# Performance work log

Hardware: AMD Instinct MI355X
Metric: run time of the kernel (lower is better)

The kernel has to match this reference:

```python
import jax, jax.numpy as jnp
import numpy as np

B, S, N, IN_DIM = 64, 12, 170, 1
E, L, C, H, OUT = 128, 4, 2, 8, 1
OFFSET, PAD = 0, 1          # seq_offset=0 -> Conv2d padding (0,1)
LOOKUP, MAXLEN = 0, 100
EPS = 1e-5


def _shift(x, s):
    """y[:, i] = x[:, i+s] along axis 1, zero padded."""
    if s == 0:
        return x
    z = jnp.zeros_like(x[:, :abs(s)])
    if s > 0:
        return jnp.concatenate([x[:, s:], z], axis=1)
    return jnp.concatenate([z, x[:, :s]], axis=1)


def _masked_conv_diag(x, w):
    """Diagonal of Conv2d(kernel=(1,3), pad=(0,PAD)) applied to the causally
    masked repeated tensor, computed directly without the O(B*S*S*E) blowup:
      out[b,i] = sum_k W[:,:,k] @ (mask(i, i+k-PAD) * x[b, i+k-PAD])
    where mask(i,j) = (j <= i) or (j < OFFSET)."""
    i = jnp.arange(x.shape[1])
    out = None
    for k in range(3):
        s = k - PAD
        term = jnp.einsum('bse,oe->bso', _shift(x, s), w[:, :, k])
        if s > 0:  # only future taps can be masked out
            term = term * (i + s < OFFSET).astype(x.dtype)[None, :, None]
        out = term if out is None else out + term
    return out


def _conv1d_k3(x, w, b):
    """Conv1d over the seq dim, kernel 3, padding 1, with bias. x:[b,s,e]."""
    out = b
    for k in range(3):
        out = out + jnp.einsum('bse,oe->bso', _shift(x, k - 1), w[:, :, k])
    return out


def _layer_norm(x, g, b):
    m = jnp.mean(x, -1, keepdims=True)
    v = jnp.mean((x - m) ** 2, -1, keepdims=True)
    return (x - m) * jax.lax.rsqrt(v + EPS) * g + b


def _mha(q_in, kv_in, w, b, mask=None):
    dh = E // H
    q = (q_in @ w[0] + b[0]).reshape(q_in.shape[0], q_in.shape[1], H, dh)
    k = (kv_in @ w[1] + b[1]).reshape(kv_in.shape[0], kv_in.shape[1], H, dh)
    v = (kv_in @ w[2] + b[2]).reshape(kv_in.shape[0], kv_in.shape[1], H, dh)
    s = jnp.einsum('bqhd,bkhd->bhqk', q, k) * np.float32(1.0 / np.sqrt(dh))
    if mask is not None:
        s = jnp.where(mask[None, None], s, jnp.float32(-1e9))
    a = jax.nn.softmax(s, axis=-1)
    o = jnp.einsum('bhqk,bkhd->bqhd', a, v).reshape(q_in.shape[0], q_in.shape[1], E)
    return o @ w[3] + b[3]


def setup_inputs() -> dict:
    key = jax.random.key(0)
    ks = jax.random.split(key, 16)

    def nrm(k, shape, scale=0.05):
        return scale * jax.random.normal(k, shape, dtype=jnp.float32)

    # sinusoidal positional table, length MAXLEN
    pos = np.arange(MAXLEN)[:, None].astype(np.float32)
    div = np.exp(-np.log(10000.0) * np.arange(0, E, 2) / E).astype(np.float32)
    pe = np.zeros((MAXLEN, E), np.float32)
    pe[:, 0::2] = np.sin(pos * div)
    pe[:, 1::2] = np.cos(pos * div)

    return {
        'x': jax.random.normal(ks[0], (B, S, N, IN_DIM), jnp.float32),
        'enc_x': jax.random.normal(ks[1], (C, B * N, S, E), jnp.float32),
        'tgt_mask': jnp.tril(jnp.ones((S, S), bool)),
        'emb_w': nrm(ks[2], (IN_DIM, E), 1.0),
        'emb_b': jnp.zeros((E,), jnp.float32),
        'pe': jnp.asarray(pe),
        'conv_q_w': nrm(ks[3], (L, E, E, 3)),
        'conv_k_w': nrm(ks[4], (L, C, E, E, 3)),
        'conv_k_b': jnp.zeros((L, C, E), jnp.float32),
        'sa_w': nrm(ks[5], (L, 4, E, E)),
        'sa_b': jnp.zeros((L, 4, E), jnp.float32),
        'ca_w': nrm(ks[6], (L, C, 4, E, E)),
        'ca_b': jnp.zeros((L, C, 4, E), jnp.float32),
        'ff_w1': nrm(ks[7], (L, E, 4 * E)),
        'ff_b1': jnp.zeros((L, 4 * E), jnp.float32),
        'ff_w2': nrm(ks[8], (L, 4 * E, E)),
        'ff_b2': jnp.zeros((L, E), jnp.float32),
        'ln_g': jnp.ones((L, 3, E), jnp.float32),
        'ln_b': jnp.zeros((L, 3, E), jnp.float32),
        'fc_w': nrm(ks[9], (E, OUT)),
        'fc_b': jnp.zeros((OUT,), jnp.float32),
    }


def reference(x, enc_x, tgt_mask, emb_w, emb_b, pe, conv_q_w, conv_k_w, conv_k_b,
              sa_w, sa_b, ca_w, ca_b, ff_w1, ff_b1, ff_w2, ff_b2, ln_g, ln_b,
              fc_w, fc_b):
    h = x @ emb_w + emb_b                                    # [B,S,N,E]
    h = jnp.transpose(h, (1, 0, 2, 3)).reshape(S, B * N, E)  # [S,B*N,E]
    h = jnp.transpose(h, (1, 0, 2))                          # [B*N,S,E]
    h = h + pe[LOOKUP:LOOKUP + S]
    for l in range(L):
        # local trends: causal masked-conv query (the fused diagonal)
        h = _masked_conv_diag(h, conv_q_w[l])
        enc_list = [_conv1d_k3(enc_x[i], conv_k_w[l, i], conv_k_b[l, i])
                    for i in range(C)]
        # decoder block: self-attn -> cross-attn (avg over features) -> FFN
        h = _layer_norm(h + _mha(h, h, sa_w[l], sa_b[l], tgt_mask),
                        ln_g[l, 0], ln_b[l, 0])
        cross = sum(_mha(h, enc_list[i], ca_w[l, i], ca_b[l, i])
                    for i in range(C)) / C
        h = _layer_norm(h + cross, ln_g[l, 1], ln_b[l, 1])
        f = jax.nn.relu(h @ ff_w1[l] + ff_b1[l]) @ ff_w2[l] + ff_b2[l]
        h = _layer_norm(h + f, ln_g[l, 2], ln_b[l, 2])
    out = h @ fc_w + fc_b                                    # [B*N,S,OUT]
    out = jnp.transpose(out, (1, 0, 2)).reshape(S, B, N, OUT)
    return jnp.transpose(out, (1, 0, 2, 3))                  # [B,S,N,OUT]
```

## Files before the change

### kernel.cpp

```cpp
#include <hip/hip_runtime.h>


#define B_   64
#define S_   12
#define N_   170
#define BN_  (B_*N_)
#define E_   128
#define L_   4
#define C_   2
#define H_   8
#define DH_  16
#define FF_  512
#define EPS_ 1e-5f
#define THREADS 256

typedef unsigned short u16;
typedef __attribute__((ext_vector_type(4))) float f32x4;
typedef __attribute__((ext_vector_type(8))) u16   us8;
typedef __attribute__((ext_vector_type(4))) u16   us4;
typedef __attribute__((ext_vector_type(8))) __bf16 bf16x8;
union FragU { us8 u; bf16x8 b; };

__device__ __forceinline__ u16 f2bf(float f) {
    __bf16 h = (__bf16)f;
    return __builtin_bit_cast(u16, h);
}
__device__ __forceinline__ float bf2f(u16 s) {
    return __builtin_bit_cast(float, (unsigned)s << 16);
}

__global__ void k_wpack(const float* __restrict__ cq, const float* __restrict__ sa,
                        const float* __restrict__ ck, const float* __restrict__ ca,
                        const float* __restrict__ f1, const float* __restrict__ f2,
                        u16* __restrict__ wp) {
    int f  = blockIdx.x * 256 + threadIdx.x;
    int l  = f / 57344, fl = f % 57344;
    const float* src; int sk, so, KS, q;
    if (fl < 4096)        { int tap = fl >> 11; q = fl & 2047; KS = 4;
                            src = cq + (size_t)l*49152 + tap;            sk = 3;   so = 384; }
    else if (fl < 12288)  { int j = (fl - 4096) >> 11; q = fl & 2047; KS = 4;
                            src = sa + (size_t)(l*4 + j)*16384;          sk = 128; so = 1;   }
    else if (fl < 24576)  { int ct = (fl - 12288) >> 11; q = fl & 2047; KS = 4;
                            int ci = ct / 3, tap = ct % 3;
                            src = ck + (size_t)(l*2 + ci)*49152 + tap;   sk = 3;   so = 384; }
    else if (fl < 40960)  { int cj = (fl - 24576) >> 11; q = fl & 2047; KS = 4;
                            src = ca + (size_t)(l*8 + cj)*16384;         sk = 128; so = 1;   }
    else if (fl < 49152)  { q = fl - 40960; KS = 4;
                            src = f1 + (size_t)l*65536;                  sk = 512; so = 1;   }
    else                  { q = fl - 49152; KS = 16;
                            src = f2 + (size_t)l*65536;                  sk = 128; so = 1;   }
    int lane = q & 63, tt = q >> 6;
    int ks = tt % KS, ntile = tt / KS;
    int k0 = ks*32 + ((lane >> 4) << 3);
    int o  = ntile*16 + (lane & 15);
    us8 w;
    #pragma unroll
    for (int i = 0; i < 8; i++) w[i] = f2bf(src[(size_t)(k0 + i)*sk + (size_t)o*so]);
    *(us8*)(wp + (size_t)f*8) = w;
}

__device__ __forceinline__ void stage24(const float* __restrict__ src, u16* dst, int t) {
    #pragma unroll
    for (int it = 0; it < 3; it++) {
        int i = t + it*THREADS;
        const f32x4 v = ((const f32x4*)src)[i];
        int elem = i << 2;
        int srow = elem >> 7;
        int g = srow / 12, s = srow - g*12;
        int row = g*16 + s;
        int colb = (elem & 127) << 1;
        us4 w; w[0] = f2bf(v[0]); w[1] = f2bf(v[1]); w[2] = f2bf(v[2]); w[3] = f2bf(v[3]);
        *(us4*)((char*)dst + (((row << 8) + colb) ^ ((row & 7) << 4))) = w;
    }
}

__device__ __forceinline__ void stage24_embed(const float* __restrict__ x,
    const float* __restrict__ ew, const float* __restrict__ eb,
    const float* __restrict__ pe, int bn0, u16* dst, int t) {
    #pragma unroll
    for (int it = 0; it < 3; it++) {
        int i = t + it*THREADS;
        int elem = i << 2;
        int srow = elem >> 7;
        int g = srow / 12, s = srow - g*12;
        int row = g*16 + s;
        int col = elem & 127;
        int bn = bn0 + g, b = bn / N_, n = bn - b*N_;
        float xv = x[(b*S_ + s)*N_ + n];
        const f32x4 w  = *(const f32x4*)(ew + col);
        const f32x4 bb = *(const f32x4*)(eb + col);
        const f32x4 p  = *(const f32x4*)(pe + s*E_ + col);
        us4 o; o[0] = f2bf(xv*w[0] + bb[0] + p[0]); o[1] = f2bf(xv*w[1] + bb[1] + p[1]);
               o[2] = f2bf(xv*w[2] + bb[2] + p[2]); o[3] = f2bf(xv*w[3] + bb[3] + p[3]);
        *(us4*)((char*)dst + (((row << 8) + (col << 1)) ^ ((row & 7) << 4))) = o;
    }
}

__device__ __forceinline__ void acc_init(f32x4 (&acc)[2][2], const float* bias, int wave, int lane) {
    #pragma unroll
    for (int nt = 0; nt < 2; nt++) {
        float bv = bias ? bias[(wave*2 + nt)*16 + (lane & 15)] : 0.f;
        #pragma unroll
        for (int mt = 0; mt < 2; mt++) {
            acc[mt][nt][0] = bv; acc[mt][nt][1] = bv; acc[mt][nt][2] = bv; acc[mt][nt][3] = bv;
        }
    }
}

__device__ __forceinline__ bf16x8 ldA(const u16* A, int row, int colb) {
    FragU fu; fu.u = *(const us8*)((const char*)A + (((row << 8) + colb) ^ ((row & 7) << 4)));
    return fu.b;
}

template<int KSTOT>
__device__ __forceinline__ void gemm24(const u16* A, const us8* __restrict__ WP, int ksOff,
                                       f32x4 (&acc)[2][2], int wave, int lane) {
    #pragma unroll
    for (int ks = 0; ks < 4; ks++) {
        int colb = (ks*32 + ((lane >> 4) << 3)) << 1;
        bf16x8 a[2];
        #pragma unroll
        for (int mt = 0; mt < 2; mt++) a[mt] = ldA(A, mt*16 + (lane & 15), colb);
        #pragma unroll
        for (int nt = 0; nt < 2; nt++) {
            FragU fb; fb.u = WP[((wave*2 + nt)*KSTOT + ksOff + ks)*64 + lane];
            #pragma unroll
            for (int mt = 0; mt < 2; mt++)
                acc[mt][nt] = __builtin_amdgcn_mfma_f32_16x16x32_bf16(a[mt], fb.b, acc[mt][nt], 0, 0, 0);
        }
    }
}

__device__ __forceinline__ void gemm24_rows(const u16* A, const u16* ZR, const int (&sr)[2],
                                            const us8* __restrict__ WP,
                                            f32x4 (&acc)[2][2], int wave, int lane) {
    #pragma unroll
    for (int ks = 0; ks < 4; ks++) {
        int colb = (ks*32 + ((lane >> 4) << 3)) << 1;
        bf16x8 a[2];
        #pragma unroll
        for (int mt = 0; mt < 2; mt++) {
            const char* p = (sr[mt] >= 0)
                ? (const char*)A + (((sr[mt] << 8) + colb) ^ ((sr[mt] & 7) << 4))
                : (const char*)ZR + colb;
            FragU fu; fu.u = *(const us8*)p;
            a[mt] = fu.b;
        }
        #pragma unroll
        for (int nt = 0; nt < 2; nt++) {
            FragU fb; fb.u = WP[((wave*2 + nt)*4 + ks)*64 + lane];
            #pragma unroll
            for (int mt = 0; mt < 2; mt++)
                acc[mt][nt] = __builtin_amdgcn_mfma_f32_16x16x32_bf16(a[mt], fb.b, acc[mt][nt], 0, 0, 0);
        }
    }
}

__device__ __forceinline__ void gemm24_x3(const u16* A,
        const us8* __restrict__ B0, const us8* __restrict__ B1, const us8* __restrict__ B2,
        f32x4 (&c0)[2][2], f32x4 (&c1)[2][2], f32x4 (&c2)[2][2], int wave, int lane) {
    #pragma unroll
    for (int ks = 0; ks < 4; ks++) {
        int colb = (ks*32 + ((lane >> 4) << 3)) << 1;
        bf16x8 a[2];
        #pragma unroll
        for (int mt = 0; mt < 2; mt++) a[mt] = ldA(A, mt*16 + (lane & 15), colb);
        #pragma unroll
        for (int nt = 0; nt < 2; nt++) {
            int bi = ((wave*2 + nt)*4 + ks)*64 + lane;
            FragU f0, f1, f2; f0.u = B0[bi]; f1.u = B1[bi]; f2.u = B2[bi];
            #pragma unroll
            for (int mt = 0; mt < 2; mt++) {
                c0[mt][nt] = __builtin_amdgcn_mfma_f32_16x16x32_bf16(a[mt], f0.b, c0[mt][nt], 0, 0, 0);
                c1[mt][nt] = __builtin_amdgcn_mfma_f32_16x16x32_bf16(a[mt], f1.b, c1[mt][nt], 0, 0, 0);
                c2[mt][nt] = __builtin_amdgcn_mfma_f32_16x16x32_bf16(a[mt], f2.b, c2[mt][nt], 0, 0, 0);
            }
        }
    }
}

__device__ __forceinline__ void gemm24_x2(const u16* A,
        const us8* __restrict__ B0, const us8* __restrict__ B1,
        f32x4 (&c0)[2][2], f32x4 (&c1)[2][2], int wave, int lane) {
    #pragma unroll
    for (int ks = 0; ks < 4; ks++) {
        int colb = (ks*32 + ((lane >> 4) << 3)) << 1;
        bf16x8 a[2];
        #pragma unroll
        for (int mt = 0; mt < 2; mt++) a[mt] = ldA(A, mt*16 + (lane & 15), colb);
        #pragma unroll
        for (int nt = 0; nt < 2; nt++) {
            int bi = ((wave*2 + nt)*4 + ks)*64 + lane;
            FragU f0, f1; f0.u = B0[bi]; f1.u = B1[bi];
            #pragma unroll
            for (int mt = 0; mt < 2; mt++) {
                c0[mt][nt] = __builtin_amdgcn_mfma_f32_16x16x32_bf16(a[mt], f0.b, c0[mt][nt], 0, 0, 0);
                c1[mt][nt] = __builtin_amdgcn_mfma_f32_16x16x32_bf16(a[mt], f1.b, c1[mt][nt], 0, 0, 0);
            }
        }
    }
}

template<bool RELU>
__device__ __forceinline__ void acc_store_bf(const f32x4 (&acc)[2][2], u16* Bp, int wave, int lane) {
    #pragma unroll
    for (int mt = 0; mt < 2; mt++)
    #pragma unroll
    for (int nt = 0; nt < 2; nt++)
    #pragma unroll
    for (int r = 0; r < 4; r++) {
        int row = mt*16 + ((lane >> 4) << 2) + r;
        int col = (wave*2 + nt)*16 + (lane & 15);
        float v = acc[mt][nt][r];
        if (RELU) v = fmaxf(v, 0.f);
        *(u16*)((char*)Bp + (((row << 8) + (col << 1)) ^ ((row & 7) << 4))) = f2bf(v);
    }
}

__device__ __forceinline__ void ld16(const u16* Bf, int row, int colb, float* o16) {
    int x = (row & 7) << 4;
    int base = (row << 8) + colb;
    us8 u0 = *(const us8*)((const char*)Bf + (base ^ x));
    us8 u1 = *(const us8*)((const char*)Bf + ((base + 16) ^ x));
    #pragma unroll
    for (int d = 0; d < 8; d++) { o16[d] = bf2f(u0[d]); o16[8+d] = bf2f(u1[d]); }
}

template<bool MASK>
__device__ __forceinline__ void attn24(u16* QA, const u16* KB, const u16* VB, int t) {
    if (t < 192) {
        int g = t / 96, rem = t % 96;
        int hh = rem / 12, qi = rem % 12;
        int hb2 = hh << 5;
        int rq = g*16 + qi;
        float qv[16]; ld16(QA, rq, hb2, qv);
        float sc[12]; float mx = -1e30f;
        #pragma unroll
        for (int j = 0; j < 12; j++) {
            float kv[16]; ld16(KB, g*16 + j, hb2, kv);
            float s = 0.f;
            #pragma unroll
            for (int d = 0; d < 16; d++) s += qv[d]*kv[d];
            s *= 0.25f;
            if (MASK && j > qi) s = -1e30f;
            sc[j] = s; mx = fmaxf(mx, s);
        }
        float sum = 0.f;
        #pragma unroll
        for (int j = 0; j < 12; j++) { sc[j] = __expf(sc[j] - mx); sum += sc[j]; }
        float inv = 1.f/sum;
        float ov[16];
        #pragma unroll
        for (int d = 0; d < 16; d++) ov[d] = 0.f;
        #pragma unroll
        for (int j = 0; j < 12; j++) {
            float vv[16]; ld16(VB, g*16 + j, hb2, vv);
            #pragma unroll
            for (int d = 0; d < 16; d++) ov[d] += sc[j]*vv[d];
        }
        int x = (rq & 7) << 4;
        us8 w0, w1;
        #pragma unroll
        for (int d = 0; d < 8; d++) { w0[d] = f2bf(ov[d]*inv); w1[d] = f2bf(ov[8+d]*inv); }
        *(us8*)((char*)QA + (((rq << 8) + hb2) ^ x))      = w0;
        *(us8*)((char*)QA + (((rq << 8) + hb2 + 16) ^ x)) = w1;
    }
}

__device__ __forceinline__ void ln_inreg(f32x4 (&v)[2][2], float* lnbuf,
                                         const float* __restrict__ g, const float* __restrict__ bb,
                                         int wave, int lane) {
    float gc[2], bc[2];
    #pragma unroll
    for (int nt = 0; nt < 2; nt++) {
        int col = (wave*2 + nt)*16 + (lane & 15);
        gc[nt] = g[col]; bc[nt] = bb[col];
    }
    #pragma unroll
    for (int mt = 0; mt < 2; mt++)
    #pragma unroll
    for (int r = 0; r < 4; r++) {
        float a = v[mt][0][r], c = v[mt][1][r];
        float p = a + c, q = a*a + c*c;
        #pragma unroll
        for (int off = 1; off < 16; off <<= 1) { p += __shfl_xor(p, off); q += __shfl_xor(q, off); }
        if ((lane & 15) == 0) {
            int row = mt*16 + ((lane >> 4) << 2) + r;
            lnbuf[(row*4 + wave)*2]     = p;
            lnbuf[(row*4 + wave)*2 + 1] = q;
        }
    }
    __syncthreads();
    #pragma unroll
    for (int mt = 0; mt < 2; mt++)
    #pragma unroll
    for (int r = 0; r < 4; r++) {
        int row = mt*16 + ((lane >> 4) << 2) + r;
        float sum = 0.f, ss = 0.f;
        #pragma unroll
        for (int w2 = 0; w2 < 4; w2++) { sum += lnbuf[(row*4 + w2)*2]; ss += lnbuf[(row*4 + w2)*2 + 1]; }
        float m   = sum * (1.f/128.f);
        float var = ss * (1.f/128.f) - m*m;
        float inv = rsqrtf(var + EPS_);
        #pragma unroll
        for (int nt = 0; nt < 2; nt++)
            v[mt][nt][r] = (v[mt][nt][r] - m)*inv*gc[nt] + bc[nt];
    }
}

template<bool EMB, bool FIN>
__global__ void __launch_bounds__(THREADS, 2)
k_layer(float* __restrict__ h, const float* __restrict__ x,
        const float* __restrict__ ew, const float* __restrict__ ebp, const float* __restrict__ pe,
        const float* __restrict__ encx, const u16* __restrict__ lw,
        const float* __restrict__ sab, const float* __restrict__ ckb, const float* __restrict__ cab,
        const float* __restrict__ fb1, const float* __restrict__ fb2,
        const float* __restrict__ lg, const float* __restrict__ lb,
        const float* __restrict__ fcw, const float* __restrict__ fcb,
        float* __restrict__ outp) {
    __shared__ __align__(16) u16 P0[4096], P1[4096], P2[4096], P3[4096], P4[4096], ZR[128];
    __shared__ __align__(16) float lnbuf[256];

    int t = threadIdx.x, wave = t >> 6, lane = t & 63;
    int bid = blockIdx.x;
    float* hp = h + (size_t)(bid*2) * (S_*E_);

    if (t < 64) ((unsigned*)ZR)[t] = 0;
    if (EMB) stage24_embed(x, ew, ebp, pe, bid*2, P0, t);
    else     stage24(hp, P0, t);
    stage24(encx + (size_t)(bid*2) * (S_*E_), P4, t);
    __syncthreads();

    int rr = lane & 15;
    int srp[2], srf[2], srn[2];
    #pragma unroll
    for (int mt = 0; mt < 2; mt++) {
        srp[mt] = (rr >= 1)     ? mt*16 + rr - 1 : -1;
        srf[mt] = mt*16 + rr;
        srn[mt] = (rr + 1 < 12) ? mt*16 + rr + 1 : -1;
    }

    f32x4 cacc[2][2];
    acc_init(cacc, nullptr, wave, lane);
    gemm24_rows(P0, ZR, srp, (const us8*)lw,           cacc, wave, lane);
    gemm24_rows(P0, ZR, srf, (const us8*)(lw + 16384), cacc, wave, lane);
    acc_store_bf<false>(cacc, P1, wave, lane);
    __syncthreads();

    {
        const us8* sap = (const us8*)(lw + 32768);
        f32x4 aq[2][2], ak[2][2], av[2][2];
        acc_init(aq, sab,       wave, lane);
        acc_init(ak, sab + 128, wave, lane);
        acc_init(av, sab + 256, wave, lane);
        gemm24_x3(P1, sap, sap + 2048, sap + 4096, aq, ak, av, wave, lane);
        acc_store_bf<false>(aq, P0, wave, lane);
        acc_store_bf<false>(ak, P2, wave, lane);
        acc_store_bf<false>(av, P3, wave, lane);
    }
    __syncthreads();
    attn24<true>(P0, P2, P3, t);
    __syncthreads();

    f32x4 hres[2][2];
    {
        f32x4 a[2][2];
        acc_init(a, sab + 384, wave, lane);
        gemm24<4>(P0, (const us8*)(lw + 81920), 0, a, wave, lane);
        #pragma unroll
        for (int mt = 0; mt < 2; mt++)
        #pragma unroll
        for (int nt = 0; nt < 2; nt++) hres[mt][nt] = a[mt][nt] + cacc[mt][nt];
    }
    ln_inreg(hres, lnbuf, lg, lb, wave, lane);
    acc_store_bf<false>(hres, P1, wave, lane);
    __syncthreads();

    f32x4 creg[2][2];
    #pragma unroll
    for (int nt = 0; nt < 2; nt++) {
        int col = (wave*2 + nt)*16 + (lane & 15);
        float bv = cab[3*128 + col] + cab[7*128 + col];
        #pragma unroll
        for (int mt = 0; mt < 2; mt++) { creg[mt][nt][0]=bv; creg[mt][nt][1]=bv; creg[mt][nt][2]=bv; creg[mt][nt][3]=bv; }
    }

    {
        const us8* ckp = (const us8*)(lw + 98304);
        f32x4 a[2][2];
        acc_init(a, ckb, wave, lane);
        gemm24_rows(P4, ZR, srp, ckp,        a, wave, lane);
        gemm24_rows(P4, ZR, srf, ckp + 2048, a, wave, lane);
        gemm24_rows(P4, ZR, srn, ckp + 4096, a, wave, lane);
        acc_store_bf<false>(a, P3, wave, lane);
    }
    __syncthreads();
    const us8* cap0 = (const us8*)(lw + 196608);
    {
        f32x4 aq[2][2], ak[2][2], av[2][2];
        acc_init(aq, cab, wave, lane);
        gemm24<4>(P1, cap0, 0, aq, wave, lane);
        acc_store_bf<false>(aq, P0, wave, lane);
        acc_init(ak, cab + 128, wave, lane);
        acc_init(av, cab + 256, wave, lane);
        gemm24_x2(P3, cap0 + 2048, cap0 + 4096, ak, av, wave, lane);
        acc_store_bf<false>(ak, P2, wave, lane);
        acc_store_bf<false>(av, P4, wave, lane);
    }
    __syncthreads();
    stage24(encx + ((size_t)BN_ + bid*2) * (S_*E_), P3, t);
    attn24<false>(P0, P2, P4, t);
    __syncthreads();
    gemm24<4>(P0, cap0 + 6144, 0, creg, wave, lane);
    __syncthreads();

    {
        const us8* ckp = (const us8*)(lw + 98304 + 3*16384);
        f32x4 a[2][2];
        acc_init(a, ckb + 128, wave, lane);
        gemm24_rows(P3, ZR, srp, ckp,        a, wave, lane);
        gemm24_rows(P3, ZR, srf, ckp + 2048, a, wave, lane);
        gemm24_rows(P3, ZR, srn, ckp + 4096, a, wave, lane);
        acc_store_bf<false>(a, P0, wave, lane);
    }
    __syncthreads();
    const us8* cap1 = (const us8*)(lw + 196608 + 4*16384);
    {
        f32x4 aq[2][2], ak[2][2], av[2][2];
        acc_init(aq, cab + 4*128, wave, lane);
        gemm24<4>(P1, cap1, 0, aq, wave, lane);
        acc_store_bf<false>(aq, P2, wave, lane);
        acc_init(ak, cab + 5*128, wave, lane);
        acc_init(av, cab + 6*128, wave, lane);
        gemm24_x2(P0, cap1 + 2048, cap1 + 4096, ak, av, wave, lane);
        acc_store_bf<false>(ak, P3, wave, lane);
        acc_store_bf<false>(av, P4, wave, lane);
    }
    __syncthreads();
    attn24<false>(P2, P3, P4, t);
    __syncthreads();
    gemm24<4>(P2, cap1 + 6144, 0, creg, wave, lane);

    #pragma unroll
    for (int mt = 0; mt < 2; mt++)
    #pragma unroll
    for (int nt = 0; nt < 2; nt++) hres[mt][nt] = hres[mt][nt] + 0.5f*creg[mt][nt];
    __syncthreads();
    ln_inreg(hres, lnbuf, lg + 128, lb + 128, wave, lane);
    acc_store_bf<false>(hres, P1, wave, lane);
    __syncthreads();

    f32x4 ffacc[2][2];
    acc_init(ffacc, fb2, wave, lane);
    #pragma unroll
    for (int c = 0; c < 4; c++) {
        u16* MB = (c & 1) ? P3 : P2;
        {
            f32x4 a[2][2];
            acc_init(a, fb1 + c*128, wave, lane);
            gemm24<4>(P1, (const us8*)(lw + 327680) + c*2048, 0, a, wave, lane);
            acc_store_bf<true>(a, MB, wave, lane);
        }
        __syncthreads();
        gemm24<16>(MB, (const us8*)(lw + 393216), c*4, ffacc, wave, lane);
    }
    #pragma unroll
    for (int mt = 0; mt < 2; mt++)
    #pragma unroll
    for (int nt = 0; nt < 2; nt++) hres[mt][nt] = hres[mt][nt] + ffacc[mt][nt];
    ln_inreg(hres, lnbuf, lg + 256, lb + 256, wave, lane);

    if (FIN) {
        float fw[2];
        #pragma unroll
        for (int nt = 0; nt < 2; nt++) fw[nt] = fcw[(wave*2 + nt)*16 + (lane & 15)];
        float pr[2][4];
        #pragma unroll
        for (int mt = 0; mt < 2; mt++)
        #pragma unroll
        for (int r = 0; r < 4; r++) {
            float p = hres[mt][0][r]*fw[0] + hres[mt][1][r]*fw[1];
            #pragma unroll
            for (int off = 1; off < 16; off <<= 1) p += __shfl_xor(p, off);
            pr[mt][r] = p;
        }
        __syncthreads();
        if ((lane & 15) == 0) {
            #pragma unroll
            for (int mt = 0; mt < 2; mt++)
            #pragma unroll
            for (int r = 0; r < 4; r++) {
                int row = mt*16 + ((lane >> 4) << 2) + r;
                lnbuf[row*4 + wave] = pr[mt][r];
            }
        }
        __syncthreads();
        if (t < 24) {
            int g = t / 12, s = t % 12;
            int row = g*16 + s;
            float s4 = lnbuf[row*4] + lnbuf[row*4+1] + lnbuf[row*4+2] + lnbuf[row*4+3] + fcb[0];
            int bn = bid*2 + g;
            int b = bn / N_, n = bn - b*N_;
            outp[(b*S_ + s)*N_ + n] = s4;
        }
    } else {
        #pragma unroll
        for (int mt = 0; mt < 2; mt++)
        #pragma unroll
        for (int r = 0; r < 4; r++) {
            int row = ((lane >> 4) << 2) + r;
            if (row < 12) {
                #pragma unroll
                for (int nt = 0; nt < 2; nt++) {
                    int col = (wave*2 + nt)*16 + (lane & 15);
                    hp[(mt*S_ + row)*E_ + col] = hres[mt][nt][r];
                }
            }
        }
    }
}

extern "C" void kernel_launch(void* const* d_in, const int* in_sizes, int n_in,
                              void* d_out, int out_size, void* d_ws, size_t ws_size,
                              hipStream_t stream) {
    const float* x        = (const float*)d_in[0];
    const float* enc_x    = (const float*)d_in[1];
    const float* emb_w    = (const float*)d_in[3];
    const float* emb_b    = (const float*)d_in[4];
    const float* pe       = (const float*)d_in[5];
    const float* conv_q_w = (const float*)d_in[6];
    const float* conv_k_w = (const float*)d_in[7];
    const float* conv_k_b = (const float*)d_in[8];
    const float* sa_w     = (const float*)d_in[9];
    const float* sa_b     = (const float*)d_in[10];
    const float* ca_w     = (const float*)d_in[11];
    const float* ca_b     = (const float*)d_in[12];
    const float* ff_w1    = (const float*)d_in[13];
    const float* ff_b1    = (const float*)d_in[14];
    const float* ff_w2    = (const float*)d_in[15];
    const float* ff_b2    = (const float*)d_in[16];
    const float* ln_g     = (const float*)d_in[17];
    const float* ln_b     = (const float*)d_in[18];
    const float* fc_w     = (const float*)d_in[19];
    const float* fc_b     = (const float*)d_in[20];

    const size_t HN = (size_t)BN_ * S_ * E_;
    float* h  = (float*)d_ws;
    u16* wpk  = (u16*)((float*)d_ws + HN);

    k_wpack<<<896, 256, 0, stream>>>(conv_q_w, sa_w, conv_k_w, ca_w, ff_w1, ff_w2, wpk);

    for (int l = 0; l < L_; l++) {
        const u16* lw = wpk + (size_t)l*458752;
        const float* sab = sa_b + l*512;
        const float* ckb = conv_k_b + l*256;
        const float* cab = ca_b + l*1024;
        const float* fb1 = ff_b1 + l*512;
        const float* fb2 = ff_b2 + l*128;
        const float* lg  = ln_g + l*384;
        const float* lb  = ln_b + l*384;
        if (l == 0)
            k_layer<true, false><<<BN_/2, THREADS, 0, stream>>>(h, x, emb_w, emb_b, pe, enc_x, lw,
                sab, ckb, cab, fb1, fb2, lg, lb, fc_w, fc_b, (float*)d_out);
        else if (l == L_-1)
            k_layer<false, true><<<BN_/2, THREADS, 0, stream>>>(h, x, emb_w, emb_b, pe, enc_x, lw,
                sab, ckb, cab, fb1, fb2, lg, lb, fc_w, fc_b, (float*)d_out);
        else
            k_layer<false, false><<<BN_/2, THREADS, 0, stream>>>(h, x, emb_w, emb_b, pe, enc_x, lw,
                sab, ckb, cab, fb1, fb2, lg, lb, fc_w, fc_b, (float*)d_out);
    }
}
```

Baseline: 1.546 ms.

## Store inter-layer activations and encoder inputs in bf16 and drop zero-row buffer

The hidden state passed between layer kernels is now stored as bf16 rather than fp32. Encoder inputs are converted to bf16 once by a new pre-pass kernel, so each layer stages half the bytes from global memory. Out-of-range conv taps now read explicitly zeroed pad rows in shared memory instead of a separate zero buffer, and lnbuf is aliased into P2 to reduce shared memory. This adds a conversion pass over enc_x and rounds the residual stream to bf16 between layers, which may cost accuracy.

```diff
diff --git a/kernel.cpp b/kernel.cpp
--- a/kernel.cpp
+++ b/kernel.cpp
@@ -27,6 +27,18 @@
 }
 __device__ __forceinline__ float bf2f(u16 s) {
     return __builtin_bit_cast(float, (unsigned)s << 16);
+}
+
+__global__ void k_encbf(const float* __restrict__ src, u16* __restrict__ dst, int n8) {
+    int i = blockIdx.x * 256 + threadIdx.x;
+    if (i < n8) {
+        const f32x4 v0 = ((const f32x4*)src)[i*2];
+        const f32x4 v1 = ((const f32x4*)src)[i*2 + 1];
+        us8 w;
+        w[0]=f2bf(v0[0]); w[1]=f2bf(v0[1]); w[2]=f2bf(v0[2]); w[3]=f2bf(v0[3]);
+        w[4]=f2bf(v1[0]); w[5]=f2bf(v1[1]); w[6]=f2bf(v1[2]); w[7]=f2bf(v1[3]);
+        ((us8*)dst)[i] = w;
+    }
 }
 
 __global__ void k_wpack(const float* __restrict__ cq, const float* __restrict__ sa,
@@ -59,19 +71,25 @@
     *(us8*)(wp + (size_t)f*8) = w;
 }
 
-__device__ __forceinline__ void stage24(const float* __restrict__ src, u16* dst, int t) {
-    #pragma unroll
-    for (int it = 0; it < 3; it++) {
-        int i = t + it*THREADS;
-        const f32x4 v = ((const f32x4*)src)[i];
-        int elem = i << 2;
-        int srow = elem >> 7;
-        int g = srow / 12, s = srow - g*12;
-        int row = g*16 + s;
-        int colb = (elem & 127) << 1;
-        us4 w; w[0] = f2bf(v[0]); w[1] = f2bf(v[1]); w[2] = f2bf(v[2]); w[3] = f2bf(v[3]);
-        *(us4*)((char*)dst + (((row << 8) + colb) ^ ((row & 7) << 4))) = w;
-    }
+__device__ __forceinline__ void zero_pad_rows(u16* dst, int t) {
+    if (t < 128) {
+        int chunk = t & 15, ridx = t >> 4;
+        int row = 12 + (ridx & 3) + ((ridx >> 2) << 4);
+        us8 z = {0,0,0,0,0,0,0,0};
+        *(us8*)((char*)dst + (((row << 8) + (chunk << 4)) ^ ((row & 7) << 4))) = z;
+    }
+}
+
+__device__ __forceinline__ void stage24_bf(const u16* __restrict__ src, u16* dst, int t) {
+    for (int i = t; i < 384; i += THREADS) {
+        us8 v = ((const us8*)src)[i];
+        int row = i >> 4;
+        int g = row / 12, s = row - g*12;
+        int rowT = g*16 + s;
+        int colb = (i & 15) << 4;
+        *(us8*)((char*)dst + (((rowT << 8) + colb) ^ ((rowT & 7) << 4))) = v;
+    }
+    zero_pad_rows(dst, t);
 }
 
 __device__ __forceinline__ void stage24_embed(const float* __restrict__ x,
@@ -94,6 +112,7 @@
                o[2] = f2bf(xv*w[2] + bb[2] + p[2]); o[3] = f2bf(xv*w[3] + bb[3] + p[3]);
         *(us4*)((char*)dst + (((row << 8) + (col << 1)) ^ ((row & 7) << 4))) = o;
     }
+    zero_pad_rows(dst, t);
 }
 
 __device__ __forceinline__ void acc_init(f32x4 (&acc)[2][2], const float* bias, int wave, int lane) {
@@ -131,7 +150,7 @@
     }
 }
 
-__device__ __forceinline__ void gemm24_rows(const u16* A, const u16* ZR, const int (&sr)[2],
+__device__ __forceinline__ void gemm24_rows(const u16* A, const int (&sr)[2],
                                             const us8* __restrict__ WP,
                                             f32x4 (&acc)[2][2], int wave, int lane) {
     #pragma unroll
@@ -139,13 +158,7 @@
         int colb = (ks*32 + ((lane >> 4) << 3)) << 1;
         bf16x8 a[2];
         #pragma unroll
-        for (int mt = 0; mt < 2; mt++) {
-            const char* p = (sr[mt] >= 0)
-                ? (const char*)A + (((sr[mt] << 8) + colb) ^ ((sr[mt] & 7) << 4))
-                : (const char*)ZR + colb;
-            FragU fu; fu.u = *(const us8*)p;
-            a[mt] = fu.b;
-        }
+        for (int mt = 0; mt < 2; mt++) a[mt] = ldA(A, sr[mt], colb);
         #pragma unroll
         for (int nt = 0; nt < 2; nt++) {
             FragU fb; fb.u = WP[((wave*2 + nt)*4 + ks)*64 + lane];
@@ -310,40 +323,39 @@
 
 template<bool EMB, bool FIN>
 __global__ void __launch_bounds__(THREADS, 2)
-k_layer(float* __restrict__ h, const float* __restrict__ x,
+k_layer(u16* __restrict__ hb, const float* __restrict__ x,
         const float* __restrict__ ew, const float* __restrict__ ebp, const float* __restrict__ pe,
-        const float* __restrict__ encx, const u16* __restrict__ lw,
+        const u16* __restrict__ encb, const u16* __restrict__ lw,
         const float* __restrict__ sab, const float* __restrict__ ckb, const float* __restrict__ cab,
         const float* __restrict__ fb1, const float* __restrict__ fb2,
         const float* __restrict__ lg, const float* __restrict__ lb,
         const float* __restrict__ fcw, const float* __restrict__ fcb,
         float* __restrict__ outp) {
-    __shared__ __align__(16) u16 P0[4096], P1[4096], P2[4096], P3[4096], P4[4096], ZR[128];
-    __shared__ __align__(16) float lnbuf[256];
+    __shared__ __align__(16) u16 P0[4096], P1[4096], P2[4096], P3[4096], P4[4096];
+    float* lnbuf = (float*)P2;
 
     int t = threadIdx.x, wave = t >> 6, lane = t & 63;
     int bid = blockIdx.x;
-    float* hp = h + (size_t)(bid*2) * (S_*E_);
-
-    if (t < 64) ((unsigned*)ZR)[t] = 0;
+    u16* hp = hb + (size_t)(bid*2) * (S_*E_);
+
     if (EMB) stage24_embed(x, ew, ebp, pe, bid*2, P0, t);
-    else     stage24(hp, P0, t);
-    stage24(encx + (size_t)(bid*2) * (S_*E_), P4, t);
+    else     stage24_bf(hp, P0, t);
+    stage24_bf(encb + (size_t)(bid*2) * (S_*E_), P4, t);
     __syncthreads();
 
     int rr = lane & 15;
     int srp[2], srf[2], srn[2];
     #pragma unroll
     for (int mt = 0; mt < 2; mt++) {
-        srp[mt] = (rr >= 1)     ? mt*16 + rr - 1 : -1;
+        srp[mt] = (rr >= 1)     ? mt*16 + rr - 1 : mt*16 + 12;
         srf[mt] = mt*16 + rr;
-        srn[mt] = (rr + 1 < 12) ? mt*16 + rr + 1 : -1;
+        srn[mt] = (rr + 1 < 12) ? mt*16 + rr + 1 : mt*16 + 12;
     }
 
     f32x4 cacc[2][2];
     acc_init(cacc, nullptr, wave, lane);
-    gemm24_rows(P0, ZR, srp, (const us8*)lw,           cacc, wave, lane);
-    gemm24_rows(P0, ZR, srf, (const us8*)(lw + 16384), cacc, wave, lane);
+    gemm24_rows(P0, srp, (const us8*)lw,           cacc, wave, lane);
+    gemm24_rows(P0, srf, (const us8*)(lw + 16384), cacc, wave, lane);
     acc_store_bf<false>(cacc, P1, wave, lane);
     __syncthreads();
 
@@ -389,9 +401,9 @@
         const us8* ckp = (const us8*)(lw + 98304);
         f32x4 a[2][2];
         acc_init(a, ckb, wave, lane);
-        gemm24_rows(P4, ZR, srp, ckp,        a, wave, lane);
-        gemm24_rows(P4, ZR, srf, ckp + 2048, a, wave, lane);
-        gemm24_rows(P4, ZR, srn, ckp + 4096, a, wave, lane);
+        gemm24_rows(P4, srp, ckp,        a, wave, lane);
+        gemm24_rows(P4, srf, ckp + 2048, a, wave, lane);
+        gemm24_rows(P4, srn, ckp + 4096, a, wave, lane);
         acc_store_bf<false>(a, P3, wave, lane);
     }
     __syncthreads();
@@ -408,7 +420,7 @@
         acc_store_bf<false>(av, P4, wave, lane);
     }
     __syncthreads();
-    stage24(encx + ((size_t)BN_ + bid*2) * (S_*E_), P3, t);
+    stage24_bf(encb + ((size_t)BN_ + bid*2) * (S_*E_), P3, t);
     attn24<false>(P0, P2, P4, t);
     __syncthreads();
     gemm24<4>(P0, cap0 + 6144, 0, creg, wave, lane);
@@ -418,9 +430,9 @@
         const us8* ckp = (const us8*)(lw + 98304 + 3*16384);
         f32x4 a[2][2];
         acc_init(a, ckb + 128, wave, lane);
-        gemm24_rows(P3, ZR, srp, ckp,        a, wave, lane);
-        gemm24_rows(P3, ZR, srf, ckp + 2048, a, wave, lane);
-        gemm24_rows(P3, ZR, srn, ckp + 4096, a, wave, lane);
+        gemm24_rows(P3, srp, ckp,        a, wave, lane);
+        gemm24_rows(P3, srf, ckp + 2048, a, wave, lane);
+        gemm24_rows(P3, srn, ckp + 4096, a, wave, lane);
         acc_store_bf<false>(a, P0, wave, lane);
     }
     __syncthreads();
@@ -513,7 +525,7 @@
                 #pragma unroll
                 for (int nt = 0; nt < 2; nt++) {
                     int col = (wave*2 + nt)*16 + (lane & 15);
-                    hp[(mt*S_ + row)*E_ + col] = hres[mt][nt][r];
+                    hp[(mt*S_ + row)*E_ + col] = f2bf(hres[mt][nt][r]);
                 }
             }
         }
@@ -545,9 +557,14 @@
     const float* fc_b     = (const float*)d_in[20];
 
     const size_t HN = (size_t)BN_ * S_ * E_;
-    float* h  = (float*)d_ws;
-    u16* wpk  = (u16*)((float*)d_ws + HN);
-
+    u16* hb   = (u16*)d_ws;
+    u16* encb = hb + HN;
+    u16* wpk  = encb + 2*HN;
+
+    {
+        int n8 = (int)(2*HN/8);
+        k_encbf<<<(n8 + 255)/256, 256, 0, stream>>>(enc_x, encb, n8);
+    }
     k_wpack<<<896, 256, 0, stream>>>(conv_q_w, sa_w, conv_k_w, ca_w, ff_w1, ff_w2, wpk);
 
     for (int l = 0; l < L_; l++) {
@@ -560,13 +577,13 @@
         const float* lg  = ln_g + l*384;
         const float* lb  = ln_b + l*384;
         if (l == 0)
-            k_layer<true, false><<<BN_/2, THREADS, 0, stream>>>(h, x, emb_w, emb_b, pe, enc_x, lw,
+            k_layer<true, false><<<BN_/2, THREADS, 0, stream>>>(hb, x, emb_w, emb_b, pe, encb, lw,
                 sab, ckb, cab, fb1, fb2, lg, lb, fc_w, fc_b, (float*)d_out);
         else if (l == L_-1)
-            k_layer<false, true><<<BN_/2, THREADS, 0, stream>>>(h, x, emb_w, emb_b, pe, enc_x, lw,
+            k_layer<false, true><<<BN_/2, THREADS, 0, stream>>>(hb, x, emb_w, emb_b, pe, encb, lw,
                 sab, ckb, cab, fb1, fb2, lg, lb, fc_w, fc_b, (float*)d_out);
         else
-            k_layer<false, false><<<BN_/2, THREADS, 0, stream>>>(h, x, emb_w, emb_b, pe, enc_x, lw,
+            k_layer<false, false><<<BN_/2, THREADS, 0, stream>>>(hb, x, emb_w, emb_b, pe, encb, lw,
                 sab, ckb, cab, fb1, fb2, lg, lb, fc_w, fc_b, (float*)d_out);
     }
 }
```

New measurement: 1.551 ms. About the same (+0.3%).
